# Performance work log

Measured on AMD Instinct MI355X. Metric: run time of the kernel, lower is better.

Reference implementation:

```python
import jax, jax.numpy as jnp
import numpy as np

B, S = 4096, 4096
NS, FDIM = 16, 64


def _ln(x, g, b):
    mu = jnp.mean(x, axis=-1, keepdims=True)
    v = jnp.mean((x - mu) ** 2, axis=-1, keepdims=True)
    return (x - mu) / jnp.sqrt(v + 1e-5) * g + b


def _rolling_vol_mean(returns, w):
    # mean over all length-w windows of unbiased std (matches per-window torch.std loop)
    Bn, L = returns.shape
    z = jnp.zeros((Bn, 1), returns.dtype)
    c1 = jnp.concatenate([z, jnp.cumsum(returns, axis=1)], axis=1)
    c2 = jnp.concatenate([z, jnp.cumsum(returns * returns, axis=1)], axis=1)
    s = c1[:, w:] - c1[:, :-w]    # [B, L-w+1] window sums
    s2 = c2[:, w:] - c2[:, :-w]
    var = (s2 - s * s / w) / (w - 1)
    return jnp.mean(jnp.sqrt(jnp.maximum(var, 0.0)), axis=1, keepdims=True)


def setup_inputs() -> dict:
    key = jax.random.key(0)
    ks = jax.random.split(key, 24)
    r = lambda i, shp: jax.random.normal(ks[i], shp, jnp.float32) * 0.05
    return {
        'price_series': jax.random.uniform(ks[0], (B, S, 1), jnp.float32) * 10.0 + 1.0,
        're_W': r(1, (4, 4, 64)), 're_b': r(2, (4, 64)),
        're_g': jnp.ones((4, 64), jnp.float32), 're_beta': jnp.zeros((4, 64), jnp.float32),
        'rh_W1': r(3, (256, 64)), 'rh_b1': r(4, (64,)), 'rh_W2': r(5, (64, 4)), 'rh_b2': r(6, (4,)),
        'rv_W': r(7, (3, 128)), 'rv_b': r(8, (128,)),
        'rv_g': jnp.ones((128,), jnp.float32), 'rv_beta': jnp.zeros((128,), jnp.float32),
        'vs_W': r(9, (128, 128)), 'vs_b': r(10, (128,)),
        'vs_g': jnp.ones((128,), jnp.float32), 'vs_beta': jnp.zeros((128,), jnp.float32),
        'vc_W1': r(11, (256, 64)), 'vc_b1': r(12, (64,)), 'vc_W2': r(13, (64, 4)), 'vc_b2': r(14, (4,)),
        'emb': r(15, (NS, FDIM)),
        'cn_W1': r(16, (576, 128)), 'cn_b1': r(17, (128,)),
        'cn_W2': r(18, (128, 64)), 'cn_b2': r(19, (64,)),
        'cn_W3': r(20, (64, 1)), 'cn_b3': r(21, (1,)),
    }


def reference(price_series, re_W, re_b, re_g, re_beta, rh_W1, rh_b1, rh_W2, rh_b2,
              rv_W, rv_b, rv_g, rv_beta, vs_W, vs_b, vs_g, vs_beta,
              vc_W1, vc_b1, vc_W2, vc_b2, emb, cn_W1, cn_b1, cn_W2, cn_b2, cn_W3, cn_b3):
    prices = price_series[:, :, 0]            # [B,S]
    Bn, Sn = prices.shape
    # --- MarketRegimeEncoder: SMA-20 via prefix sums (the per-step torch loop) ---
    cs = jnp.cumsum(prices, axis=1)
    shifted = jnp.concatenate([jnp.zeros((Bn, 20), prices.dtype), cs[:, :-20]], axis=1)
    counts = jnp.minimum(jnp.arange(Sn) + 1, 20).astype(prices.dtype)
    sma20 = (cs - shifted) / counts           # (sma_5 is computed but unused in original)
    trend = jnp.mean((prices - sma20) / (sma20 + 1e-8), axis=1, keepdims=True)
    p10 = prices[:, Sn - 10:Sn - 9]
    momentum = (prices[:, -1:] - p10) / (p10 + 1e-8)
    pmean = jnp.mean(prices, axis=1, keepdims=True)
    mean_rev = (prices[:, -1:] - pmean) / (pmean + 1e-8)
    pstd = jnp.std(prices, axis=1, keepdims=True, ddof=1)
    cycle = pstd / (pmean + 1e-8)
    combined = jnp.concatenate([trend, momentum, mean_rev, cycle], axis=1)  # [B,4]
    h = jax.nn.relu(jnp.einsum('bi,kio->bko', combined, re_W) + re_b[None])  # [B,4,64]
    h = _ln(h, re_g[None], re_beta[None])
    regime_features = h.reshape(Bn, -1)        # [B,256] (trend|momentum|mean_rev|cycle)
    logits = jax.nn.relu(regime_features @ rh_W1 + rh_b1) @ rh_W2 + rh_b2
    regime_probs = jax.nn.softmax(logits, axis=1)
    # --- VolatilityEncodingModule ---
    logp = jnp.log(jnp.maximum(price_series, 1e-8))
    returns = jnp.diff(logp, axis=1)[:, :, 0]  # [B,S-1]
    vol_in = jnp.concatenate([_rolling_vol_mean(returns, w) for w in (5, 10, 20)], axis=1)  # [B,3]
    rv = _ln(jax.nn.relu(vol_in @ rv_W + rv_b), rv_g, rv_beta)
    vs = _ln(jax.nn.relu(rv @ vs_W + vs_b), vs_g, vs_beta)
    vol_features = jnp.concatenate([rv, vs], axis=1)  # [B,256]
    vlogits = jax.nn.relu(vol_features @ vc_W1 + vc_b1) @ vc_W2 + vc_b2
    vol_regime = jax.nn.softmax(vlogits, axis=1)
    # --- OptionsStrategyEncoder: vectorized over strategies ---
    mv = jnp.concatenate([regime_features, vol_features], axis=1)  # [B,512]
    mvp = mv @ cn_W1[:512]                    # [B,128]
    ep = emb @ cn_W1[512:]                    # [NS,128]
    h1 = jax.nn.relu(mvp[:, None, :] + ep[None, :, :] + cn_b1)  # [B,NS,128]
    h2 = jax.nn.relu(h1 @ cn_W2 + cn_b2)      # [B,NS,64]
    scores = (h2 @ cn_W3 + cn_b3)[:, :, 0]    # [B,NS]
    return regime_features, regime_probs, vol_features, vol_regime, scores
```

## Files before the change

kernel.cpp:

```cpp
#include <hip/hip_runtime.h>
#include <math.h>

#define NROWS 4096
#define SLEN  4096
#define RETN  4095
#define CHK   20

__global__ __launch_bounds__(256) void k_ep(const float* __restrict__ emb,
                                            const float* __restrict__ cn_W1,
                                            const float* __restrict__ cn_b1,
                                            float* __restrict__ ep) {
    int idx = blockIdx.x * 256 + threadIdx.x;
    if (idx >= 16 * 128) return;
    int n = idx >> 7, o = idx & 127;
    float acc = cn_b1[o];
    const float* w = cn_W1 + 512 * 128;
    for (int i = 0; i < 64; ++i) acc = fmaf(emb[n * 64 + i], w[i * 128 + o], acc);
    ep[idx] = acc;
}

__global__ void k_stats(const float* __restrict__ price,
                        float* __restrict__ combined,
                        float* __restrict__ volin) {
    __shared__ float scm[260 * CHK];
    __shared__ float red[6][4];

    const int tid = threadIdx.x;
    const int row = blockIdx.x;
    const float* pr = price + (size_t)row * SLEN;

    float pA = 0.f, pB = 0.f;
    if (tid == 0) { pA = pr[SLEN - 10]; pB = pr[SLEN - 1]; }

    if (tid < 40) { scm[tid] = 0.f; scm[258 * CHK + tid] = 0.f; }

    #pragma unroll
    for (int it = 0; it < 4; ++it) {
        const int i = it * 256 + tid;
        const float4 v = ((const float4*)pr)[i];
        *(float4*)&scm[(2 + (i >> 2)) * CHK + ((4 * i) & 15)] = v;
    }
    __syncthreads();

    const int s0 = tid * 16;

    float hb[20], x_[16];
    *(float4*)&hb[0] = *(const float4*)&scm[tid * CHK + 12];
    #pragma unroll
    for (int k = 0; k < 4; ++k)
        *(float4*)&hb[4 + 4 * k] = *(const float4*)&scm[(tid + 1) * CHK + 4 * k];
    #pragma unroll
    for (int k = 0; k < 4; ++k)
        *(float4*)&x_[4 * k] = *(const float4*)&scm[(tid + 2) * CHK + 4 * k];
    const float pn = scm[(tid + 3) * CHK];

    float W = 0.f;
    #pragma unroll
    for (int k = 0; k < 20; ++k) W += hb[k];
    float st = 0.f, s1p = 0.f, s2p = 0.f;
    #pragma unroll
    for (int d = 0; d < 16; ++d) {
        const float x = x_[d];
        W += x - hb[d];
        float inv_cnt = 0.05f;
        if (s0 == 0)                 inv_cnt = 1.0f / (float)(d + 1);
        else if (s0 == 16 && d < 3)  inv_cnt = 1.0f / (float)(17 + d);
        const float sma = W * inv_cnt;
        st  = fmaf(x - sma, __builtin_amdgcn_rcpf(sma + 1e-8f), st);
        s1p += x;
        s2p = fmaf(x, x, s2p);
    }

    float lg[17];
    #pragma unroll
    for (int d = 0; d < 16; ++d) lg[d] = __builtin_amdgcn_logf(fmaxf(x_[d], 1e-8f));
    lg[16] = __builtin_amdgcn_logf(fmaxf(pn, 1e-8f));
    float rs[36];
    #pragma unroll
    for (int d = 0; d < 16; ++d) rs[d] = lg[d + 1] - lg[d];

    __syncthreads();
    #pragma unroll
    for (int k = 0; k < 4; ++k)
        *(float4*)&scm[(tid + 2) * CHK + 4 * k] = *(const float4*)&rs[4 * k];
    __syncthreads();

    #pragma unroll
    for (int k = 0; k < 4; ++k)
        *(float4*)&rs[16 + 4 * k] = *(const float4*)&scm[(tid + 3) * CHK + 4 * k];
    *(float4*)&rs[32] = *(const float4*)&scm[(tid + 4) * CHK];

    float S5 = 0.f, Q5 = 0.f, S10 = 0.f, Q10 = 0.f, S20 = 0.f, Q20 = 0.f;
    #pragma unroll
    for (int j = 0; j < 20; ++j) {
        const float x = rs[j];
        S20 += x; Q20 = fmaf(x, x, Q20);
        if (j < 10) { S10 += x; Q10 = fmaf(x, x, Q10); }
        if (j < 5)  { S5  += x; Q5  = fmaf(x, x, Q5); }
    }

    #define SQT(S, Q, invw) \
        __builtin_amdgcn_sqrtf(fmaxf(fmaf(-(S) * (invw), (S), (Q)), 0.f))

    float v5 = 0.f, v10 = 0.f, v20 = 0.f;
    if (tid < 254) {
        #pragma unroll
        for (int d = 0; d < 16; ++d) {
            v5  += SQT(S5,  Q5,  0.2f);
            v10 += SQT(S10, Q10, 0.1f);
            v20 += SQT(S20, Q20, 0.05f);
            const float xo = rs[d], qo = xo * xo;
            const float a5 = rs[d + 5], a10 = rs[d + 10], a20 = rs[d + 20];
            S5  += a5  - xo;  Q5  = fmaf(a5,  a5,  Q5)  - qo;
            S10 += a10 - xo;  Q10 = fmaf(a10, a10, Q10) - qo;
            S20 += a20 - xo;  Q20 = fmaf(a20, a20, Q20) - qo;
        }
    } else {
        #pragma unroll
        for (int d = 0; d < 16; ++d) {
            const int i = s0 + d;
            if (i < 4091) v5  += SQT(S5,  Q5,  0.2f);
            if (i < 4086) v10 += SQT(S10, Q10, 0.1f);
            if (i < 4076) v20 += SQT(S20, Q20, 0.05f);
            const float xo = rs[d], qo = xo * xo;
            const float a5 = rs[d + 5], a10 = rs[d + 10], a20 = rs[d + 20];
            S5  += a5  - xo;  Q5  = fmaf(a5,  a5,  Q5)  - qo;
            S10 += a10 - xo;  Q10 = fmaf(a10, a10, Q10) - qo;
            S20 += a20 - xo;  Q20 = fmaf(a20, a20, Q20) - qo;
        }
    }
    #undef SQT

    {
        float vals[6] = {s1p, s2p, st, v5, v10, v20};
        const int lane = tid & 63, wid = tid >> 6;
        #pragma unroll
        for (int v = 0; v < 6; ++v) {
            float x = vals[v];
            for (int o = 32; o > 0; o >>= 1) x += __shfl_xor(x, o, 64);
            if (lane == 0) red[v][wid] = x;
        }
    }
    __syncthreads();
    if (tid == 0) {
        const float sum_p  = red[0][0] + red[0][1] + red[0][2] + red[0][3];
        const float sum_p2 = red[1][0] + red[1][1] + red[1][2] + red[1][3];
        const float sum_t  = red[2][0] + red[2][1] + red[2][2] + red[2][3];
        const float sv5    = red[3][0] + red[3][1] + red[3][2] + red[3][3];
        const float sv10   = red[4][0] + red[4][1] + red[4][2] + red[4][3];
        const float sv20   = red[5][0] + red[5][1] + red[5][2] + red[5][3];
        const float pmean = sum_p * (1.f / 4096.f);
        const float varp  = fmaf(-sum_p * (1.f / 4096.f), sum_p, sum_p2) * (1.f / 4095.f);
        const float pstd  = __builtin_amdgcn_sqrtf(fmaxf(varp, 0.f));
        const float ipm   = __builtin_amdgcn_rcpf(pmean + 1e-8f);
        combined[row * 4 + 0] = sum_t * (1.f / 4096.f);
        combined[row * 4 + 1] = (pB - pA) * __builtin_amdgcn_rcpf(pA + 1e-8f);
        combined[row * 4 + 2] = (pB - pmean) * ipm;
        combined[row * 4 + 3] = pstd * ipm;
        const float LN2 = 0.6931471805599453f;
        volin[row * 3 + 0] = sv5  * (LN2 * 0.5f                 / 4091.f);
        volin[row * 3 + 1] = sv10 * (LN2 * (1.f / 3.f)          / 4086.f);
        volin[row * 3 + 2] = sv20 * (LN2 * 0.22941573387056174f / 4076.f);
    }
}

__global__ __launch_bounds__(256) void k_mlp(const float* __restrict__ combined,
                                             const float* __restrict__ volin,
                                             const float* __restrict__ re_W,  const float* __restrict__ re_b,
                                             const float* __restrict__ re_g,  const float* __restrict__ re_be,
                                             const float* __restrict__ rh_W1, const float* __restrict__ rh_b1,
                                             const float* __restrict__ rh_W2, const float* __restrict__ rh_b2,
                                             const float* __restrict__ rv_W,  const float* __restrict__ rv_b,
                                             const float* __restrict__ rv_g,  const float* __restrict__ rv_be,
                                             const float* __restrict__ vs_W,  const float* __restrict__ vs_b,
                                             const float* __restrict__ vs_g,  const float* __restrict__ vs_be,
                                             const float* __restrict__ vc_W1, const float* __restrict__ vc_b1,
                                             const float* __restrict__ vc_W2, const float* __restrict__ vc_b2,
                                             float* __restrict__ out_rf, float* __restrict__ out_rp,
                                             float* __restrict__ out_vf, float* __restrict__ out_vr) {
    __shared__ float rf_lds[8][256];
    __shared__ float vf_lds[8][256];
    __shared__ float ps[4][8][64];
    __shared__ float hid_s[8][64];
    __shared__ float prt[4][8];
    __shared__ float cmb_s[8][4];
    __shared__ float vol_s[8][3];

    const int tid  = threadIdx.x;
    const int lane = tid & 63;
    const int wid  = tid >> 6;
    const int row0 = blockIdx.x * 8;

    if (tid < 32) cmb_s[tid >> 2][tid & 3] = combined[(size_t)(row0 + (tid >> 2)) * 4 + (tid & 3)];
    else if (tid < 56) { int t = tid - 32; vol_s[t / 3][t % 3] = volin[(size_t)(row0 + t / 3) * 3 + t % 3]; }
    __syncthreads();

    {
        const float* w = re_W + wid * 256;
        const float w0 = w[lane], w1 = w[64 + lane], w2 = w[128 + lane], w3 = w[192 + lane];
        const float b  = re_b[wid * 64 + lane];
        const float gg = re_g[wid * 64 + lane], bb = re_be[wid * 64 + lane];
        float h[8], sm[8], sq[8];
        #pragma unroll
        for (int r = 0; r < 8; ++r) {
            float v = fmaf(cmb_s[r][0], w0, fmaf(cmb_s[r][1], w1,
                      fmaf(cmb_s[r][2], w2, fmaf(cmb_s[r][3], w3, b))));
            h[r] = fmaxf(v, 0.f);
            sm[r] = h[r]; sq[r] = h[r] * h[r];
        }
        #pragma unroll
        for (int off = 32; off > 0; off >>= 1) {
            #pragma unroll
            for (int r = 0; r < 8; ++r) {
                sm[r] += __shfl_xor(sm[r], off, 64);
                sq[r] += __shfl_xor(sq[r], off, 64);
            }
        }
        #pragma unroll
        for (int r = 0; r < 8; ++r) {
            const float mu  = sm[r] * (1.f / 64.f);
            const float var = fmaxf(sq[r] * (1.f / 64.f) - mu * mu, 0.f);
            const float y = (h[r] - mu) * rsqrtf(var + 1e-5f) * gg + bb;
            rf_lds[r][wid * 64 + lane] = y;
            out_rf[(size_t)(row0 + r) * 256 + wid * 64 + lane] = y;
        }
    }
    __syncthreads();

    {
        const int i0 = wid * 64;
        float acc[8] = {0.f, 0.f, 0.f, 0.f, 0.f, 0.f, 0.f, 0.f};
        for (int i = 0; i < 64; ++i) {
            const float wv = rh_W1[(size_t)(i0 + i) * 64 + lane];
            #pragma unroll
            for (int r = 0; r < 8; ++r) acc[r] = fmaf(rf_lds[r][i0 + i], wv, acc[r]);
        }
        #pragma unroll
        for (int r = 0; r < 8; ++r) ps[wid][r][lane] = acc[r];
    }
    __syncthreads();

    for (int it = tid; it < 512; it += 256) {
        const int r = it >> 6, o = it & 63;
        const float v = ps[0][r][o] + ps[1][r][o] + ps[2][r][o] + ps[3][r][o] + rh_b1[o];
        hid_s[r][o] = fmaxf(v, 0.f);
    }
    __syncthreads();

    if (tid < 32) {
        const int r = tid >> 2, j = tid & 3;
        float acc = rh_b2[j];
        for (int i = 0; i < 64; ++i) acc = fmaf(hid_s[r][i], rh_W2[i * 4 + j], acc);
        float m = acc;
        m = fmaxf(m, __shfl_xor(m, 1, 64));
        m = fmaxf(m, __shfl_xor(m, 2, 64));
        const float e = expf(acc - m);
        float s = e;
        s += __shfl_xor(s, 1, 64);
        s += __shfl_xor(s, 2, 64);
        out_rp[(size_t)(row0 + r) * 4 + j] = e / s;
    }

    {
        const int o = tid & 127, g = tid >> 7, wv_ = tid >> 6;
        const float w0 = rv_W[o], w1 = rv_W[128 + o], w2 = rv_W[256 + o];
        const float b = rv_b[o], gg = rv_g[o], bb = rv_be[o];
        float h[4], sm[4], sq[4];
        #pragma unroll
        for (int r4 = 0; r4 < 4; ++r4) {
            const int r = g * 4 + r4;
            float v = fmaf(vol_s[r][0], w0, fmaf(vol_s[r][1], w1, fmaf(vol_s[r][2], w2, b)));
            h[r4] = fmaxf(v, 0.f);
            sm[r4] = h[r4]; sq[r4] = h[r4] * h[r4];
        }
        #pragma unroll
        for (int off = 32; off > 0; off >>= 1) {
            #pragma unroll
            for (int r4 = 0; r4 < 4; ++r4) {
                sm[r4] += __shfl_xor(sm[r4], off, 64);
                sq[r4] += __shfl_xor(sq[r4], off, 64);
            }
        }
        if (lane == 0) {
            #pragma unroll
            for (int r4 = 0; r4 < 4; ++r4) { prt[wv_][r4 * 2] = sm[r4]; prt[wv_][r4 * 2 + 1] = sq[r4]; }
        }
        __syncthreads();
        #pragma unroll
        for (int r4 = 0; r4 < 4; ++r4) {
            const float S = prt[2 * g][2 * r4]     + prt[2 * g + 1][2 * r4];
            const float Q = prt[2 * g][2 * r4 + 1] + prt[2 * g + 1][2 * r4 + 1];
            const float mu  = S * (1.f / 128.f);
            const float var = fmaxf(Q * (1.f / 128.f) - mu * mu, 0.f);
            const float y = (h[r4] - mu) * rsqrtf(var + 1e-5f) * gg + bb;
            vf_lds[g * 4 + r4][o] = y;
            out_vf[(size_t)(row0 + g * 4 + r4) * 256 + o] = y;
        }
    }
    __syncthreads();

    {
        const int o = tid & 127, g = tid >> 7, wv_ = tid >> 6;
        float acc[4];
        const float b = vs_b[o];
        #pragma unroll
        for (int r4 = 0; r4 < 4; ++r4) acc[r4] = b;
        for (int i = 0; i < 128; ++i) {
            const float wv = vs_W[(size_t)i * 128 + o];
            #pragma unroll
            for (int r4 = 0; r4 < 4; ++r4) acc[r4] = fmaf(vf_lds[g * 4 + r4][i], wv, acc[r4]);
        }
        const float gg = vs_g[o], bb = vs_be[o];
        float h[4], sm[4], sq[4];
        #pragma unroll
        for (int r4 = 0; r4 < 4; ++r4) {
            h[r4] = fmaxf(acc[r4], 0.f);
            sm[r4] = h[r4]; sq[r4] = h[r4] * h[r4];
        }
        #pragma unroll
        for (int off = 32; off > 0; off >>= 1) {
            #pragma unroll
            for (int r4 = 0; r4 < 4; ++r4) {
                sm[r4] += __shfl_xor(sm[r4], off, 64);
                sq[r4] += __shfl_xor(sq[r4], off, 64);
            }
        }
        __syncthreads();
        if (lane == 0) {
            #pragma unroll
            for (int r4 = 0; r4 < 4; ++r4) { prt[wv_][r4 * 2] = sm[r4]; prt[wv_][r4 * 2 + 1] = sq[r4]; }
        }
        __syncthreads();
        #pragma unroll
        for (int r4 = 0; r4 < 4; ++r4) {
            const float S = prt[2 * g][2 * r4]     + prt[2 * g + 1][2 * r4];
            const float Q = prt[2 * g][2 * r4 + 1] + prt[2 * g + 1][2 * r4 + 1];
            const float mu  = S * (1.f / 128.f);
            const float var = fmaxf(Q * (1.f / 128.f) - mu * mu, 0.f);
            const float y = (h[r4] - mu) * rsqrtf(var + 1e-5f) * gg + bb;
            vf_lds[g * 4 + r4][128 + o] = y;
            out_vf[(size_t)(row0 + g * 4 + r4) * 256 + 128 + o] = y;
        }
    }
    __syncthreads();

    {
        const int i0 = wid * 64;
        float acc[8] = {0.f, 0.f, 0.f, 0.f, 0.f, 0.f, 0.f, 0.f};
        for (int i = 0; i < 64; ++i) {
            const float wv = vc_W1[(size_t)(i0 + i) * 64 + lane];
            #pragma unroll
            for (int r = 0; r < 8; ++r) acc[r] = fmaf(vf_lds[r][i0 + i], wv, acc[r]);
        }
        #pragma unroll
        for (int r = 0; r < 8; ++r) ps[wid][r][lane] = acc[r];
    }
    __syncthreads();

    for (int it = tid; it < 512; it += 256) {
        const int r = it >> 6, o = it & 63;
        const float v = ps[0][r][o] + ps[1][r][o] + ps[2][r][o] + ps[3][r][o] + vc_b1[o];
        hid_s[r][o] = fmaxf(v, 0.f);
    }
    __syncthreads();
    if (tid < 32) {
        const int r = tid >> 2, j = tid & 3;
        float acc = vc_b2[j];
        for (int i = 0; i < 64; ++i) acc = fmaf(hid_s[r][i], vc_W2[i * 4 + j], acc);
        float m = acc;
        m = fmaxf(m, __shfl_xor(m, 1, 64));
        m = fmaxf(m, __shfl_xor(m, 2, 64));
        const float e = expf(acc - m);
        float s = e;
        s += __shfl_xor(s, 1, 64);
        s += __shfl_xor(s, 2, 64);
        out_vr[(size_t)(row0 + r) * 4 + j] = e / s;
    }
}

__global__ __launch_bounds__(512, 4) void k_cross(const float* __restrict__ rfin,
                                                  const float* __restrict__ vfin,
                                                  const float* __restrict__ cn_W1,
                                                  const float* __restrict__ cn_W2,
                                                  const float* __restrict__ cn_b2,
                                                  const float* __restrict__ cn_W3,
                                                  const float* __restrict__ cn_b3,
                                                  const float* __restrict__ ep,
                                                  float* __restrict__ scores) {
    __shared__ __align__(16) float w2s[128 * 64];
    __shared__ __align__(16) float uni[4096];
    __shared__ __align__(16) float mvs[4][512];
    __shared__ __align__(16) float mvp_s[4][128];
    __shared__ __align__(16) float epb[16][132];

    const int tid  = threadIdx.x;
    const int lane = tid & 63;
    const int wv   = tid >> 6;
    const int row0 = blockIdx.x * 4;

    {
        const int r = tid >> 7, cq = tid & 127;
        const float* src = (cq < 64)
            ? (rfin + (size_t)(row0 + r) * 256 + 4 * cq)
            : (vfin + (size_t)(row0 + r) * 256 + 4 * (cq - 64));
        *(float4*)&mvs[r][4 * cq] = *(const float4*)src;
    }
    #pragma unroll
    for (int k = 0; k < 4; ++k) {
        const int idx = k * 512 + tid;
        *(float4*)&w2s[4 * idx] = *(const float4*)(cn_W2 + 4 * idx);
    }
    {
        const int ns = tid >> 5, c4 = (tid & 31) * 4;
        *(float4*)&epb[ns][c4] = *(const float4*)(ep + ns * 128 + c4);
    }
    __syncthreads();

    {
        const int p = lane >> 5;
        const int q = lane & 31;
        float acc[4][4] = {{0.f}};
        const int ibase = wv * 64 + p;
        #pragma unroll 8
        for (int s = 0; s < 32; ++s) {
            const int i = ibase + 2 * s;
            const float4 w1v = *(const float4*)(cn_W1 + (size_t)i * 128 + 4 * q);
            const float m0 = mvs[0][i], m1 = mvs[1][i], m2 = mvs[2][i], m3 = mvs[3][i];
            acc[0][0] = fmaf(m0, w1v.x, acc[0][0]); acc[0][1] = fmaf(m0, w1v.y, acc[0][1]);
            acc[0][2] = fmaf(m0, w1v.z, acc[0][2]); acc[0][3] = fmaf(m0, w1v.w, acc[0][3]);
            acc[1][0] = fmaf(m1, w1v.x, acc[1][0]); acc[1][1] = fmaf(m1, w1v.y, acc[1][1]);
            acc[1][2] = fmaf(m1, w1v.z, acc[1][2]); acc[1][3] = fmaf(m1, w1v.w, acc[1][3]);
            acc[2][0] = fmaf(m2, w1v.x, acc[2][0]); acc[2][1] = fmaf(m2, w1v.y, acc[2][1]);
            acc[2][2] = fmaf(m2, w1v.z, acc[2][2]); acc[2][3] = fmaf(m2, w1v.w, acc[2][3]);
            acc[3][0] = fmaf(m3, w1v.x, acc[3][0]); acc[3][1] = fmaf(m3, w1v.y, acc[3][1]);
            acc[3][2] = fmaf(m3, w1v.z, acc[3][2]); acc[3][3] = fmaf(m3, w1v.w, acc[3][3]);
        }
        #pragma unroll
        for (int r = 0; r < 4; ++r) {
            #pragma unroll
            for (int k = 0; k < 4; ++k) acc[r][k] += __shfl_xor(acc[r][k], 32, 64);
        }
        if (p == 0) {
            #pragma unroll
            for (int r = 0; r < 4; ++r)
                *(float4*)&uni[wv * 512 + r * 128 + 4 * q] =
                    make_float4(acc[r][0], acc[r][1], acc[r][2], acc[r][3]);
        }
    }
    __syncthreads();

    {
        const int r = tid >> 7, c = tid & 127;
        float s = 0.f;
        #pragma unroll
        for (int w = 0; w < 8; ++w) s += uni[w * 512 + r * 128 + c];
        mvp_s[r][c] = s;
    }
    __syncthreads();

    const int ch  = tid >> 8;
    const int nst = tid & 255;
    const int ns  = nst >> 4;
    const int t   = nst & 15;
    float acc[4][4];
    #pragma unroll
    for (int r = 0; r < 4; ++r)
        #pragma unroll
        for (int k = 0; k < 4; ++k) acc[r][k] = 0.f;
    {
        const int c0 = ch * 64;
        #pragma unroll 2
        for (int cb = 0; cb < 64; cb += 4) {
            const int c = c0 + cb;
            float4 m4[4];
            #pragma unroll
            for (int r = 0; r < 4; ++r) m4[r] = *(const float4*)&mvp_s[r][c];
            const float4 e4 = *(const float4*)&epb[ns][c];
            {   const float4 w2v = *(const float4*)&w2s[(c + 0) * 64 + 4 * t];
                #pragma unroll
                for (int r = 0; r < 4; ++r) {
                    const float h = fmaxf(m4[r].x + e4.x, 0.f);
                    acc[r][0] = fmaf(h, w2v.x, acc[r][0]); acc[r][1] = fmaf(h, w2v.y, acc[r][1]);
                    acc[r][2] = fmaf(h, w2v.z, acc[r][2]); acc[r][3] = fmaf(h, w2v.w, acc[r][3]); } }
            {   const float4 w2v = *(const float4*)&w2s[(c + 1) * 64 + 4 * t];
                #pragma unroll
                for (int r = 0; r < 4; ++r) {
                    const float h = fmaxf(m4[r].y + e4.y, 0.f);
                    acc[r][0] = fmaf(h, w2v.x, acc[r][0]); acc[r][1] = fmaf(h, w2v.y, acc[r][1]);
                    acc[r][2] = fmaf(h, w2v.z, acc[r][2]); acc[r][3] = fmaf(h, w2v.w, acc[r][3]); } }
            {   const float4 w2v = *(const float4*)&w2s[(c + 2) * 64 + 4 * t];
                #pragma unroll
                for (int r = 0; r < 4; ++r) {
                    const float h = fmaxf(m4[r].z + e4.z, 0.f);
                    acc[r][0] = fmaf(h, w2v.x, acc[r][0]); acc[r][1] = fmaf(h, w2v.y, acc[r][1]);
                    acc[r][2] = fmaf(h, w2v.z, acc[r][2]); acc[r][3] = fmaf(h, w2v.w, acc[r][3]); } }
            {   const float4 w2v = *(const float4*)&w2s[(c + 3) * 64 + 4 * t];
                #pragma unroll
                for (int r = 0; r < 4; ++r) {
                    const float h = fmaxf(m4[r].w + e4.w, 0.f);
                    acc[r][0] = fmaf(h, w2v.x, acc[r][0]); acc[r][1] = fmaf(h, w2v.y, acc[r][1]);
                    acc[r][2] = fmaf(h, w2v.z, acc[r][2]); acc[r][3] = fmaf(h, w2v.w, acc[r][3]); } }
        }
    }
    __syncthreads();
    if (ch == 1) {
        #pragma unroll
        for (int r = 0; r < 4; ++r)
            *(float4*)&uni[nst * 16 + r * 4] = make_float4(acc[r][0], acc[r][1], acc[r][2], acc[r][3]);
    }
    __syncthreads();
    if (ch == 0) {
        #pragma unroll
        for (int r = 0; r < 4; ++r) {
            const float4 o = *(const float4*)&uni[nst * 16 + r * 4];
            acc[r][0] += o.x; acc[r][1] += o.y; acc[r][2] += o.z; acc[r][3] += o.w;
        }
        const float4 b2v = *(const float4*)(cn_b2 + 4 * t);
        const float4 w3v = *(const float4*)(cn_W3 + 4 * t);
        const float  b3v = cn_b3[0];
        #pragma unroll
        for (int r = 0; r < 4; ++r) {
            float s =      fmaxf(acc[r][0] + b2v.x, 0.f) * w3v.x;
            s = fmaf(fmaxf(acc[r][1] + b2v.y, 0.f), w3v.y, s);
            s = fmaf(fmaxf(acc[r][2] + b2v.z, 0.f), w3v.z, s);
            s = fmaf(fmaxf(acc[r][3] + b2v.w, 0.f), w3v.w, s);
            s += __shfl_xor(s, 1, 64);
            s += __shfl_xor(s, 2, 64);
            s += __shfl_xor(s, 4, 64);
            s += __shfl_xor(s, 8, 64);
            if (t == 0) scores[(size_t)(row0 + r) * 16 + ns] = s + b3v;
        }
    }
}

extern "C" void kernel_launch(void* const* d_in, const int* in_sizes, int n_in,
                              void* d_out, int out_size, void* d_ws, size_t ws_size,
                              hipStream_t stream) {
    (void)in_sizes; (void)n_in; (void)out_size; (void)ws_size;

    const float* price = (const float*)d_in[0];
    const float* re_W  = (const float*)d_in[1];
    const float* re_b  = (const float*)d_in[2];
    const float* re_g  = (const float*)d_in[3];
    const float* re_be = (const float*)d_in[4];
    const float* rh_W1 = (const float*)d_in[5];
    const float* rh_b1 = (const float*)d_in[6];
    const float* rh_W2 = (const float*)d_in[7];
    const float* rh_b2 = (const float*)d_in[8];
    const float* rv_W  = (const float*)d_in[9];
    const float* rv_b  = (const float*)d_in[10];
    const float* rv_g  = (const float*)d_in[11];
    const float* rv_be = (const float*)d_in[12];
    const float* vs_W  = (const float*)d_in[13];
    const float* vs_b  = (const float*)d_in[14];
    const float* vs_g  = (const float*)d_in[15];
    const float* vs_be = (const float*)d_in[16];
    const float* vc_W1 = (const float*)d_in[17];
    const float* vc_b1 = (const float*)d_in[18];
    const float* vc_W2 = (const float*)d_in[19];
    const float* vc_b2 = (const float*)d_in[20];
    const float* emb   = (const float*)d_in[21];
    const float* cn_W1 = (const float*)d_in[22];
    const float* cn_b1 = (const float*)d_in[23];
    const float* cn_W2 = (const float*)d_in[24];
    const float* cn_b2 = (const float*)d_in[25];
    const float* cn_W3 = (const float*)d_in[26];
    const float* cn_b3 = (const float*)d_in[27];

    float* out    = (float*)d_out;
    float* out_rf = out;
    float* out_rp = out_rf + 4096 * 256;
    float* out_vf = out_rp + 4096 * 4;
    float* out_vr = out_vf + 4096 * 256;
    float* out_sc = out_vr + 4096 * 4;

    float* ws       = (float*)d_ws;
    float* combined = ws;
    float* volin    = combined + 4096 * 4;
    float* ep       = volin + 4096 * 3;

    hipLaunchKernelGGL(k_ep,    dim3(8),    dim3(256), 0, stream, emb, cn_W1, cn_b1, ep);
    hipLaunchKernelGGL(k_stats, dim3(4096), dim3(256), 0, stream, price, combined, volin);
    hipLaunchKernelGGL(k_mlp,   dim3(512),  dim3(256), 0, stream, combined, volin,
                       re_W, re_b, re_g, re_be, rh_W1, rh_b1, rh_W2, rh_b2,
                       rv_W, rv_b, rv_g, rv_be, vs_W, vs_b, vs_g, vs_be,
                       vc_W1, vc_b1, vc_W2, vc_b2,
                       out_rf, out_rp, out_vf, out_vr);
    hipLaunchKernelGGL(k_cross, dim3(1024), dim3(512), 0, stream, out_rf, out_vf,
                       cn_W1, cn_W2, cn_b2, cn_W3, cn_b3, ep, out_sc);
}
```

Baseline: 101.2 us.

## Fuse cross-strategy scoring kernel into MLP kernel to reuse features in LDS

Merges the strategy-scoring kernel into the MLP kernel, so each 256-thread block of 8 rows computes the projection through the first scoring layer and the 16-strategy second layer straight from the regime and volatility features already held in LDS. This drops one launch and the global round-trip of reading rf/vf back. In exchange, LDS use per block grows a lot (W2 copy, ep buffer, wider partial sums). The scoring work now runs on 512 blocks of 256 threads instead of 1024 blocks of 512, which may lower occupancy and parallelism in that phase.

New measurement: 97.76 us, median of 3. -3.4%, faster.

```diff
diff --git a/kernel.cpp b/kernel.cpp
--- a/kernel.cpp
+++ b/kernel.cpp
@@ -164,23 +164,33 @@
     }
 }
 
-__global__ __launch_bounds__(256) void k_mlp(const float* __restrict__ combined,
-                                             const float* __restrict__ volin,
-                                             const float* __restrict__ re_W,  const float* __restrict__ re_b,
-                                             const float* __restrict__ re_g,  const float* __restrict__ re_be,
-                                             const float* __restrict__ rh_W1, const float* __restrict__ rh_b1,
-                                             const float* __restrict__ rh_W2, const float* __restrict__ rh_b2,
-                                             const float* __restrict__ rv_W,  const float* __restrict__ rv_b,
-                                             const float* __restrict__ rv_g,  const float* __restrict__ rv_be,
-                                             const float* __restrict__ vs_W,  const float* __restrict__ vs_b,
-                                             const float* __restrict__ vs_g,  const float* __restrict__ vs_be,
-                                             const float* __restrict__ vc_W1, const float* __restrict__ vc_b1,
-                                             const float* __restrict__ vc_W2, const float* __restrict__ vc_b2,
-                                             float* __restrict__ out_rf, float* __restrict__ out_rp,
-                                             float* __restrict__ out_vf, float* __restrict__ out_vr) {
-    __shared__ float rf_lds[8][256];
-    __shared__ float vf_lds[8][256];
-    __shared__ float ps[4][8][64];
+__global__ __launch_bounds__(256) void k_mc(const float* __restrict__ combined,
+                                            const float* __restrict__ volin,
+                                            const float* __restrict__ re_W,  const float* __restrict__ re_b,
+                                            const float* __restrict__ re_g,  const float* __restrict__ re_be,
+                                            const float* __restrict__ rh_W1, const float* __restrict__ rh_b1,
+                                            const float* __restrict__ rh_W2, const float* __restrict__ rh_b2,
+                                            const float* __restrict__ rv_W,  const float* __restrict__ rv_b,
+                                            const float* __restrict__ rv_g,  const float* __restrict__ rv_be,
+                                            const float* __restrict__ vs_W,  const float* __restrict__ vs_b,
+                                            const float* __restrict__ vs_g,  const float* __restrict__ vs_be,
+                                            const float* __restrict__ vc_W1, const float* __restrict__ vc_b1,
+                                            const float* __restrict__ vc_W2, const float* __restrict__ vc_b2,
+                                            const float* __restrict__ cn_W1,
+                                            const float* __restrict__ cn_W2,
+                                            const float* __restrict__ cn_b2,
+                                            const float* __restrict__ cn_W3,
+                                            const float* __restrict__ cn_b3,
+                                            const float* __restrict__ ep,
+                                            float* __restrict__ out_rf, float* __restrict__ out_rp,
+                                            float* __restrict__ out_vf, float* __restrict__ out_vr,
+                                            float* __restrict__ scores) {
+    __shared__ __align__(16) float w2s[128 * 64];
+    __shared__ __align__(16) float epb[16][132];
+    __shared__ __align__(16) float rf_lds[8][256];
+    __shared__ __align__(16) float vf_lds[8][256];
+    __shared__ __align__(16) float psx[4][8][128];
+    __shared__ __align__(16) float mvp_s[8][132];
     __shared__ float hid_s[8][64];
     __shared__ float prt[4][8];
     __shared__ float cmb_s[8][4];
@@ -191,6 +201,16 @@
     const int wid  = tid >> 6;
     const int row0 = blockIdx.x * 8;
 
+    #pragma unroll
+    for (int k = 0; k < 8; ++k) {
+        const int idx = k * 256 + tid;
+        *(float4*)&w2s[4 * idx] = *(const float4*)(cn_W2 + 4 * idx);
+    }
+    {
+        const int ns = tid >> 4, c8 = (tid & 15) * 8;
+        *(float4*)&epb[ns][c8]     = *(const float4*)(ep + ns * 128 + c8);
+        *(float4*)&epb[ns][c8 + 4] = *(const float4*)(ep + ns * 128 + c8 + 4);
+    }
     if (tid < 32) cmb_s[tid >> 2][tid & 3] = combined[(size_t)(row0 + (tid >> 2)) * 4 + (tid & 3)];
     else if (tid < 56) { int t = tid - 32; vol_s[t / 3][t % 3] = volin[(size_t)(row0 + t / 3) * 3 + t % 3]; }
     __syncthreads();
@@ -236,13 +256,13 @@
             for (int r = 0; r < 8; ++r) acc[r] = fmaf(rf_lds[r][i0 + i], wv, acc[r]);
         }
         #pragma unroll
-        for (int r = 0; r < 8; ++r) ps[wid][r][lane] = acc[r];
+        for (int r = 0; r < 8; ++r) psx[wid][r][lane] = acc[r];
     }
     __syncthreads();
 
     for (int it = tid; it < 512; it += 256) {
         const int r = it >> 6, o = it & 63;
-        const float v = ps[0][r][o] + ps[1][r][o] + ps[2][r][o] + ps[3][r][o] + rh_b1[o];
+        const float v = psx[0][r][o] + psx[1][r][o] + psx[2][r][o] + psx[3][r][o] + rh_b1[o];
         hid_s[r][o] = fmaxf(v, 0.f);
     }
     __syncthreads();
@@ -353,13 +373,13 @@
             for (int r = 0; r < 8; ++r) acc[r] = fmaf(vf_lds[r][i0 + i], wv, acc[r]);
         }
         #pragma unroll
-        for (int r = 0; r < 8; ++r) ps[wid][r][lane] = acc[r];
+        for (int r = 0; r < 8; ++r) psx[wid][r][lane] = acc[r];
     }
     __syncthreads();
 
     for (int it = tid; it < 512; it += 256) {
         const int r = it >> 6, o = it & 63;
-        const float v = ps[0][r][o] + ps[1][r][o] + ps[2][r][o] + ps[3][r][o] + vc_b1[o];
+        const float v = psx[0][r][o] + psx[1][r][o] + psx[2][r][o] + psx[3][r][o] + vc_b1[o];
         hid_s[r][o] = fmaxf(v, 0.f);
     }
     __syncthreads();
@@ -376,150 +396,95 @@
         s += __shfl_xor(s, 2, 64);
         out_vr[(size_t)(row0 + r) * 4 + j] = e / s;
     }
-}
-
-__global__ __launch_bounds__(512, 4) void k_cross(const float* __restrict__ rfin,
-                                                  const float* __restrict__ vfin,
-                                                  const float* __restrict__ cn_W1,
-                                                  const float* __restrict__ cn_W2,
-                                                  const float* __restrict__ cn_b2,
-                                                  const float* __restrict__ cn_W3,
-                                                  const float* __restrict__ cn_b3,
-                                                  const float* __restrict__ ep,
-                                                  float* __restrict__ scores) {
-    __shared__ __align__(16) float w2s[128 * 64];
-    __shared__ __align__(16) float uni[4096];
-    __shared__ __align__(16) float mvs[4][512];
-    __shared__ __align__(16) float mvp_s[4][128];
-    __shared__ __align__(16) float epb[16][132];
-
-    const int tid  = threadIdx.x;
-    const int lane = tid & 63;
-    const int wv   = tid >> 6;
-    const int row0 = blockIdx.x * 4;
-
-    {
-        const int r = tid >> 7, cq = tid & 127;
-        const float* src = (cq < 64)
-            ? (rfin + (size_t)(row0 + r) * 256 + 4 * cq)
-            : (vfin + (size_t)(row0 + r) * 256 + 4 * (cq - 64));
-        *(float4*)&mvs[r][4 * cq] = *(const float4*)src;
-    }
-    #pragma unroll
-    for (int k = 0; k < 4; ++k) {
-        const int idx = k * 512 + tid;
-        *(float4*)&w2s[4 * idx] = *(const float4*)(cn_W2 + 4 * idx);
-    }
-    {
-        const int ns = tid >> 5, c4 = (tid & 31) * 4;
-        *(float4*)&epb[ns][c4] = *(const float4*)(ep + ns * 128 + c4);
-    }
     __syncthreads();
 
     {
         const int p = lane >> 5;
         const int q = lane & 31;
-        float acc[4][4] = {{0.f}};
-        const int ibase = wv * 64 + p;
+        const float* mbase = (wid < 2) ? &rf_lds[0][0] + wid * 128
+                                       : &vf_lds[0][0] + (wid - 2) * 128;
+        float acc[8][4] = {{0.f}};
         #pragma unroll 8
-        for (int s = 0; s < 32; ++s) {
-            const int i = ibase + 2 * s;
-            const float4 w1v = *(const float4*)(cn_W1 + (size_t)i * 128 + 4 * q);
-            const float m0 = mvs[0][i], m1 = mvs[1][i], m2 = mvs[2][i], m3 = mvs[3][i];
-            acc[0][0] = fmaf(m0, w1v.x, acc[0][0]); acc[0][1] = fmaf(m0, w1v.y, acc[0][1]);
-            acc[0][2] = fmaf(m0, w1v.z, acc[0][2]); acc[0][3] = fmaf(m0, w1v.w, acc[0][3]);
-            acc[1][0] = fmaf(m1, w1v.x, acc[1][0]); acc[1][1] = fmaf(m1, w1v.y, acc[1][1]);
-            acc[1][2] = fmaf(m1, w1v.z, acc[1][2]); acc[1][3] = fmaf(m1, w1v.w, acc[1][3]);
-            acc[2][0] = fmaf(m2, w1v.x, acc[2][0]); acc[2][1] = fmaf(m2, w1v.y, acc[2][1]);
-            acc[2][2] = fmaf(m2, w1v.z, acc[2][2]); acc[2][3] = fmaf(m2, w1v.w, acc[2][3]);
-            acc[3][0] = fmaf(m3, w1v.x, acc[3][0]); acc[3][1] = fmaf(m3, w1v.y, acc[3][1]);
-            acc[3][2] = fmaf(m3, w1v.z, acc[3][2]); acc[3][3] = fmaf(m3, w1v.w, acc[3][3]);
-        }
-        #pragma unroll
-        for (int r = 0; r < 4; ++r) {
+        for (int s = 0; s < 64; ++s) {
+            const int i = 2 * s + p;
+            const float4 w1v = *(const float4*)(cn_W1 + (size_t)(wid * 128 + i) * 128 + 4 * q);
+            #pragma unroll
+            for (int r = 0; r < 8; ++r) {
+                const float m = mbase[r * 256 + i];
+                acc[r][0] = fmaf(m, w1v.x, acc[r][0]);
+                acc[r][1] = fmaf(m, w1v.y, acc[r][1]);
+                acc[r][2] = fmaf(m, w1v.z, acc[r][2]);
+                acc[r][3] = fmaf(m, w1v.w, acc[r][3]);
+            }
+        }
+        #pragma unroll
+        for (int r = 0; r < 8; ++r) {
             #pragma unroll
             for (int k = 0; k < 4; ++k) acc[r][k] += __shfl_xor(acc[r][k], 32, 64);
         }
         if (p == 0) {
             #pragma unroll
-            for (int r = 0; r < 4; ++r)
-                *(float4*)&uni[wv * 512 + r * 128 + 4 * q] =
+            for (int r = 0; r < 8; ++r)
+                *(float4*)&psx[wid][r][4 * q] =
                     make_float4(acc[r][0], acc[r][1], acc[r][2], acc[r][3]);
         }
     }
     __syncthreads();
 
-    {
-        const int r = tid >> 7, c = tid & 127;
-        float s = 0.f;
-        #pragma unroll
-        for (int w = 0; w < 8; ++w) s += uni[w * 512 + r * 128 + c];
-        mvp_s[r][c] = s;
-    }
-    __syncthreads();
-
-    const int ch  = tid >> 8;
-    const int nst = tid & 255;
-    const int ns  = nst >> 4;
-    const int t   = nst & 15;
-    float acc[4][4];
-    #pragma unroll
-    for (int r = 0; r < 4; ++r)
-        #pragma unroll
-        for (int k = 0; k < 4; ++k) acc[r][k] = 0.f;
-    {
-        const int c0 = ch * 64;
+    #pragma unroll
+    for (int k = 0; k < 4; ++k) {
+        const int idx = k * 256 + tid;
+        const int r = idx >> 7, c = idx & 127;
+        mvp_s[r][c] = psx[0][r][c] + psx[1][r][c] + psx[2][r][c] + psx[3][r][c];
+    }
+    __syncthreads();
+
+    {
+        const int ns = tid >> 4;
+        const int t  = tid & 15;
+        float acc[8][4];
+        #pragma unroll
+        for (int r = 0; r < 8; ++r)
+            #pragma unroll
+            for (int k = 0; k < 4; ++k) acc[r][k] = 0.f;
+
         #pragma unroll 2
-        for (int cb = 0; cb < 64; cb += 4) {
-            const int c = c0 + cb;
-            float4 m4[4];
-            #pragma unroll
-            for (int r = 0; r < 4; ++r) m4[r] = *(const float4*)&mvp_s[r][c];
+        for (int c = 0; c < 128; c += 4) {
+            float4 m4[8];
+            #pragma unroll
+            for (int r = 0; r < 8; ++r) m4[r] = *(const float4*)&mvp_s[r][c];
             const float4 e4 = *(const float4*)&epb[ns][c];
             {   const float4 w2v = *(const float4*)&w2s[(c + 0) * 64 + 4 * t];
                 #pragma unroll
-                for (int r = 0; r < 4; ++r) {
+                for (int r = 0; r < 8; ++r) {
                     const float h = fmaxf(m4[r].x + e4.x, 0.f);
                     acc[r][0] = fmaf(h, w2v.x, acc[r][0]); acc[r][1] = fmaf(h, w2v.y, acc[r][1]);
                     acc[r][2] = fmaf(h, w2v.z, acc[r][2]); acc[r][3] = fmaf(h, w2v.w, acc[r][3]); } }
             {   const float4 w2v = *(const float4*)&w2s[(c + 1) * 64 + 4 * t];
                 #pragma unroll
-                for (int r = 0; r < 4; ++r) {
+                for (int r = 0; r < 8; ++r) {
                     const float h = fmaxf(m4[r].y + e4.y, 0.f);
                     acc[r][0] = fmaf(h, w2v.x, acc[r][0]); acc[r][1] = fmaf(h, w2v.y, acc[r][1]);
                     acc[r][2] = fmaf(h, w2v.z, acc[r][2]); acc[r][3] = fmaf(h, w2v.w, acc[r][3]); } }
             {   const float4 w2v = *(const float4*)&w2s[(c + 2) * 64 + 4 * t];
                 #pragma unroll
-                for (int r = 0; r < 4; ++r) {
+                for (int r = 0; r < 8; ++r) {
                     const float h = fmaxf(m4[r].z + e4.z, 0.f);
                     acc[r][0] = fmaf(h, w2v.x, acc[r][0]); acc[r][1] = fmaf(h, w2v.y, acc[r][1]);
                     acc[r][2] = fmaf(h, w2v.z, acc[r][2]); acc[r][3] = fmaf(h, w2v.w, acc[r][3]); } }
             {   const float4 w2v = *(const float4*)&w2s[(c + 3) * 64 + 4 * t];
                 #pragma unroll
-                for (int r = 0; r < 4; ++r) {
+                for (int r = 0; r < 8; ++r) {
                     const float h = fmaxf(m4[r].w + e4.w, 0.f);
                     acc[r][0] = fmaf(h, w2v.x, acc[r][0]); acc[r][1] = fmaf(h, w2v.y, acc[r][1]);
                     acc[r][2] = fmaf(h, w2v.z, acc[r][2]); acc[r][3] = fmaf(h, w2v.w, acc[r][3]); } }
         }
-    }
-    __syncthreads();
-    if (ch == 1) {
-        #pragma unroll
-        for (int r = 0; r < 4; ++r)
-            *(float4*)&uni[nst * 16 + r * 4] = make_float4(acc[r][0], acc[r][1], acc[r][2], acc[r][3]);
-    }
-    __syncthreads();
-    if (ch == 0) {
-        #pragma unroll
-        for (int r = 0; r < 4; ++r) {
-            const float4 o = *(const float4*)&uni[nst * 16 + r * 4];
-            acc[r][0] += o.x; acc[r][1] += o.y; acc[r][2] += o.z; acc[r][3] += o.w;
-        }
+
         const float4 b2v = *(const float4*)(cn_b2 + 4 * t);
         const float4 w3v = *(const float4*)(cn_W3 + 4 * t);
         const float  b3v = cn_b3[0];
         #pragma unroll
-        for (int r = 0; r < 4; ++r) {
+        for (int r = 0; r < 8; ++r) {
             float s =      fmaxf(acc[r][0] + b2v.x, 0.f) * w3v.x;
             s = fmaf(fmaxf(acc[r][1] + b2v.y, 0.f), w3v.y, s);
             s = fmaf(fmaxf(acc[r][2] + b2v.z, 0.f), w3v.z, s);
@@ -581,11 +546,10 @@
 
     hipLaunchKernelGGL(k_ep,    dim3(8),    dim3(256), 0, stream, emb, cn_W1, cn_b1, ep);
     hipLaunchKernelGGL(k_stats, dim3(4096), dim3(256), 0, stream, price, combined, volin);
-    hipLaunchKernelGGL(k_mlp,   dim3(512),  dim3(256), 0, stream, combined, volin,
+    hipLaunchKernelGGL(k_mc,    dim3(512),  dim3(256), 0, stream, combined, volin,
                        re_W, re_b, re_g, re_be, rh_W1, rh_b1, rh_W2, rh_b2,
                        rv_W, rv_b, rv_g, rv_be, vs_W, vs_b, vs_g, vs_be,
                        vc_W1, vc_b1, vc_W2, vc_b2,
-                       out_rf, out_rp, out_vf, out_vr);
-    hipLaunchKernelGGL(k_cross, dim3(1024), dim3(512), 0, stream, out_rf, out_vf,
-                       cn_W1, cn_W2, cn_b2, cn_W3, cn_b3, ep, out_sc);
+                       cn_W1, cn_W2, cn_b2, cn_W3, cn_b3, ep,
+                       out_rf, out_rp, out_vf, out_vr, out_sc);
 }
```
